# Performance work log

Measured on AMD Instinct MI355X. Metric: run time of the kernel, lower is better.

Reference implementation:

```python
import jax, jax.numpy as jnp
import numpy as np

B = 16; Hp = 24; Wp = 24; N = Hp * Wp + 2  # 578 = patches + cls + freq tokens
D = 768; H = 12; HDIM = D // H
BAND = 64; SD = 16  # sd = min(16, max(4, band_dim))
HID = 3072  # int(embed_dim * mlp_ratio)
SCALE = HDIM ** -0.5; CLIP = 10.0
FILM_SCALE = 0.5; SPEC_INIT = 0.02; GATE_INIT = 0.05


def _ln(x, w, b, eps=1e-6):
    m = jnp.mean(x, axis=-1, keepdims=True)
    v = jnp.mean((x - m) ** 2, axis=-1, keepdims=True)
    return (x - m) * jax.lax.rsqrt(v + eps) * w + b


def _rms(x, eps=1e-6):
    return x * jax.lax.rsqrt(jnp.mean(x * x, axis=-1, keepdims=True) + eps)


def setup_inputs() -> dict:
    key = jax.random.key(0)
    ks = jax.random.split(key, 16)
    rn = lambda k, s, sc=1.0: jax.random.normal(k, s, dtype=jnp.float32) * sc
    return {
        "x": rn(ks[0], (B, N, D)),
        "band_tokens": rn(ks[1], (B, 1, D)),  # unused by forward (matches torch signature)
        "freq_token_for_cond": rn(ks[2], (B, 1, D)),
        "freq_summary": rn(ks[3], (B, D)),
        "token_band_feat": rn(ks[4], (B, N, BAND)),
        "alpha": jnp.ones((1,), jnp.float32),
        "ln_gate_w": jnp.ones((D,), jnp.float32), "ln_gate_b": jnp.zeros((D,), jnp.float32),
        "film_w": rn(ks[5], (D, 2 * D), 1e-4), "film_b": jnp.zeros((2 * D,), jnp.float32),
        "ln_attn_w": jnp.ones((D,), jnp.float32), "ln_attn_b": jnp.zeros((D,), jnp.float32),
        "qkv_w": rn(ks[6], (D, 3 * D), 0.02), "qkv_b": jnp.zeros((3 * D,), jnp.float32),
        "proj_w": rn(ks[7], (D, D), 0.02), "proj_b": jnp.zeros((D,), jnp.float32),
        "spec_bias_scale": jnp.float32(SPEC_INIT),
        "gate_w": rn(ks[8], (D, H), 1e-4), "gate_b": jnp.zeros((H,), jnp.float32),
        "band_proj_w": rn(ks[9], (BAND, SD), 0.02),
        "ln_mlp_w": jnp.ones((D,), jnp.float32), "ln_mlp_b": jnp.zeros((D,), jnp.float32),
        "fc1_w": rn(ks[10], (D, HID), 0.02), "fc1_b": jnp.zeros((HID,), jnp.float32),
        "fc2_w": rn(ks[11], (HID, D), 0.02), "fc2_b": jnp.zeros((D,), jnp.float32),
        "dw_w": rn(ks[12], (HID, 1, 3, 3), 0.1), "dw_b": jnp.zeros((HID,), jnp.float32),
    }


def _forward(x, band_tokens, freq_token_for_cond, freq_summary, token_band_feat, alpha,
             ln_gate_w, ln_gate_b, film_w, film_b, ln_attn_w, ln_attn_b,
             qkv_w, qkv_b, proj_w, proj_b, spec_bias_scale, gate_w, gate_b, band_proj_w,
             ln_mlp_w, ln_mlp_b, fc1_w, fc1_b, fc2_w, fc2_b, dw_w, dw_b):
    a = alpha.reshape(())
    # --- FiLM gate on patch tokens (replaces patch, no residual) ---
    cls_freq = x[:, :2]
    patch = x[:, 2:]
    p = _ln(patch, ln_gate_w, ln_gate_b)
    gb = freq_summary @ film_w + film_b            # [B, 2D]
    gamma, beta = jnp.split(gb, 2, axis=-1)
    gamma = jnp.tanh(gamma) * FILM_SCALE
    beta = jnp.tanh(beta) * FILM_SCALE
    patch = p * (1.0 + a * gamma[:, None, :]) + a * beta[:, None, :]
    x = jnp.concatenate([cls_freq, patch], axis=1)
    # --- spectral-similarity attention ---
    xn = _ln(x, ln_attn_w, ln_attn_b)
    qkv = (xn @ qkv_w + qkv_b).reshape(B, N, 3, H, HDIM)
    q = _rms(qkv[:, :, 0].transpose(0, 2, 1, 3))   # [B,H,N,hd]
    k = _rms(qkv[:, :, 1].transpose(0, 2, 1, 3))
    v = qkv[:, :, 2].transpose(0, 2, 1, 3)
    logits = jnp.einsum('bhnd,bhmd->bhnm', q * SCALE, k)
    s = _rms(token_band_feat @ band_proj_w)        # [B,N,SD]
    ssim = jnp.einsum('bns,bms->bnm', s, s)        # [B,N,N]
    logits = jnp.clip(logits + a * spec_bias_scale * ssim[:, None], -CLIP, CLIP)
    attn = jax.nn.softmax(logits, axis=-1)
    out = jnp.einsum('bhnm,bhmd->bhnd', attn, v)
    g = jnp.tanh(freq_token_for_cond[:, 0] @ gate_w + gate_b) * GATE_INIT  # [B,H]
    out = out * (1.0 + a * g[:, :, None, None])
    out = out.transpose(0, 2, 1, 3).reshape(B, N, D)
    x = x + (out @ proj_w + proj_b)
    # --- conv MLP on patch tokens only ---
    cls_freq = x[:, :2]
    patch = x[:, 2:]
    h = jax.nn.gelu(_ln(patch, ln_mlp_w, ln_mlp_b) @ fc1_w + fc1_b, approximate=False)
    h = h.transpose(0, 2, 1).reshape(B, HID, Hp, Wp)
    h = jax.lax.conv_general_dilated(h, dw_w, (1, 1), 'SAME', feature_group_count=HID,
                                     dimension_numbers=('NCHW', 'OIHW', 'NCHW'))
    h = jax.nn.silu(h + dw_b[None, :, None, None])
    h = h.reshape(B, HID, Hp * Wp).transpose(0, 2, 1)
    patch = patch + (h @ fc2_w + fc2_b)
    return jnp.concatenate([cls_freq, patch], axis=1)


def reference(x, band_tokens, freq_token_for_cond, freq_summary, token_band_feat, alpha,
              ln_gate_w, ln_gate_b, film_w, film_b, ln_attn_w, ln_attn_b,
              qkv_w, qkv_b, proj_w, proj_b, spec_bias_scale, gate_w, gate_b, band_proj_w,
              ln_mlp_w, ln_mlp_b, fc1_w, fc1_b, fc2_w, fc2_b, dw_w, dw_b):
    return _forward(x, band_tokens, freq_token_for_cond, freq_summary, token_band_feat, alpha,
                    ln_gate_w, ln_gate_b, film_w, film_b, ln_attn_w, ln_attn_b,
                    qkv_w, qkv_b, proj_w, proj_b, spec_bias_scale, gate_w, gate_b, band_proj_w,
                    ln_mlp_w, ln_mlp_b, fc1_w, fc1_b, fc2_w, fc2_b, dw_w, dw_b)
```

## Files before the change

### kernel.cpp

```cpp
#include <hip/hip_runtime.h>
#include <hip/hip_bf16.h>

#define BATCH 16
#define NTOK 578
#define NTOKP 592
#define NP 576
#define PGRID 24
#define DIM 768
#define NH 12
#define HDIM 64
#define BAND 64
#define SDIM 16
#define HID 3072
#define SCALE 0.125f
#define CLIPV 10.0f
#define KHS 104
#define VTS 72
#define PLS 72

typedef __attribute__((ext_vector_type(8))) short bf16x8;
typedef __attribute__((ext_vector_type(4))) float f32x4;

__device__ __forceinline__ float b2f(short u) {
  union { float f; unsigned int i; } x;
  x.i = ((unsigned int)(unsigned short)u) << 16;
  return x.f;
}
__device__ __forceinline__ short f2b(float x) {
  __hip_bfloat16 h = __float2bfloat16(x);
  return *reinterpret_cast<short*>(&h);
}

__device__ __forceinline__ void gload16(const short* g, short* l) {
  __builtin_amdgcn_global_load_lds(
      (const __attribute__((address_space(1))) unsigned int*)g,
      (__attribute__((address_space(3))) unsigned int*)l, 16, 0, 0);
}

__device__ __forceinline__ int swz_wgid(int orig, int nwg) {
  int xcd = orig & 7, i = orig >> 3;
  int q = nwg >> 3, r = nwg & 7;
  return (xcd < r) ? xcd * (q + 1) + i : r * (q + 1) + (xcd - r) * q + i;
}

__device__ __forceinline__ void block_reduce2(float& a, float& b) {
  __shared__ float sm[8];
  #pragma unroll
  for (int o = 32; o > 0; o >>= 1) { a += __shfl_down(a, o); b += __shfl_down(b, o); }
  int lane = threadIdx.x & 63, w = threadIdx.x >> 6;
  __syncthreads();
  if (lane == 0) { sm[w] = a; sm[4 + w] = b; }
  __syncthreads();
  a = sm[0] + sm[1] + sm[2] + sm[3];
  b = sm[4] + sm[5] + sm[6] + sm[7];
}

__device__ __forceinline__ void tw_body(
    const float* __restrict__ W, short* __restrict__ Wt, int K, int N,
    int kblk, int nblk, float (*t)[33]) {
  int k0 = kblk * 32, n0 = nblk * 32;
  int tx = threadIdx.x & 31, ty = threadIdx.x >> 5;
  #pragma unroll
  for (int i = 0; i < 4; i++)
    t[ty + 8 * i][tx] = W[(size_t)(k0 + ty + 8 * i) * N + n0 + tx];
  __syncthreads();
  #pragma unroll
  for (int i = 0; i < 4; i++)
    Wt[(size_t)(n0 + ty + 8 * i) * K + k0 + tx] = f2b(t[tx][ty + 8 * i]);
}

__global__ __launch_bounds__(256) void prep_weights(
    const float* __restrict__ qkv_w, const float* __restrict__ proj_w,
    const float* __restrict__ fc1_w, const float* __restrict__ fc2_w,
    const float* __restrict__ dww,
    short* __restrict__ qkvT, short* __restrict__ projT,
    short* __restrict__ fc1T, short* __restrict__ fc2T, float* __restrict__ dwt) {
  __shared__ float t[32][33];
  int id = blockIdx.x;
  if (id < 1728) {
    tw_body(qkv_w, qkvT, 768, 2304, id % 24, id / 24, t);
  } else if (id < 2304) {
    int u = id - 1728; tw_body(proj_w, projT, 768, 768, u % 24, u / 24, t);
  } else if (id < 4608) {
    int u = id - 2304; tw_body(fc1_w, fc1T, 768, 3072, u % 24, u / 24, t);
  } else if (id < 6912) {
    int u = id - 4608; tw_body(fc2_w, fc2T, 3072, 768, u % 96, u / 96, t);
  } else {
    int i = (id - 6912) * 256 + threadIdx.x;
    if (i < 9 * HID) { int tt = i / HID, c = i - tt * HID; dwt[i] = dww[c * 9 + tt]; }
  }
}

__global__ __launch_bounds__(256) void transpose_v(
    const short* __restrict__ v, short* __restrict__ vT) {
  __shared__ short t[64][72];
  int bh = blockIdx.y;
  int n0 = blockIdx.x * 64;
  int tid = threadIdx.x;
  const short* vb = v + (size_t)bh * NTOK * HDIM;
  short* ob = vT + (size_t)bh * HDIM * NTOKP;
  {
    int r = tid >> 2, c0 = (tid & 3) * 16;
    int n = n0 + r;
    bf16x8 a0 = {0,0,0,0,0,0,0,0}, a1 = {0,0,0,0,0,0,0,0};
    if (n < NTOK) {
      a0 = *(const bf16x8*)(vb + (size_t)n * HDIM + c0);
      a1 = *(const bf16x8*)(vb + (size_t)n * HDIM + c0 + 8);
    }
    *(bf16x8*)(&t[r][c0]) = a0;
    *(bf16x8*)(&t[r][c0 + 8]) = a1;
  }
  __syncthreads();
  {
    int d = tid & 63, nc = tid >> 6;
    int nbase = n0 + nc * 16;
    short tmp[16];
    #pragma unroll
    for (int e = 0; e < 16; e++) tmp[e] = t[nc * 16 + e][d];
    if (nbase + 16 <= NTOK) {
      *(bf16x8*)(ob + (size_t)d * NTOKP + nbase) = *(bf16x8*)tmp;
      *(bf16x8*)(ob + (size_t)d * NTOKP + nbase + 8) = *(bf16x8*)(tmp + 8);
    } else {
      for (int e = 0; e < 16; e++)
        if (nbase + e < NTOK) ob[(size_t)d * NTOKP + nbase + e] = tmp[e];
    }
  }
}

__global__ __launch_bounds__(256) void film_kernel(
    const float* __restrict__ fsum, const float* __restrict__ film_w, const float* __restrict__ film_b,
    const float* __restrict__ ftc, const float* __restrict__ gate_w, const float* __restrict__ gate_b,
    float* __restrict__ gamma, float* __restrict__ beta, float* __restrict__ g) {
  int bid = blockIdx.x, tid = threadIdx.x;
  if (bid < 24) {
    __shared__ float fs[BATCH][DIM];
    for (int i = tid; i < BATCH * DIM; i += 256) fs[i / DIM][i - (i / DIM) * DIM] = fsum[i];
    __syncthreads();
    int col = bid * 64 + (tid & 63);
    int b0 = tid >> 6;
    float acc[4];
    float bv = film_b[col];
    #pragma unroll
    for (int i = 0; i < 4; i++) acc[i] = bv;
    for (int k = 0; k < DIM; k++) {
      float w = film_w[(size_t)k * 2 * DIM + col];
      #pragma unroll
      for (int i = 0; i < 4; i++) acc[i] += fs[b0 + 4 * i][k] * w;
    }
    #pragma unroll
    for (int i = 0; i < 4; i++) {
      int b = b0 + 4 * i;
      float t = tanhf(acc[i]) * 0.5f;
      if (col < DIM) gamma[b * DIM + col] = t;
      else beta[b * DIM + (col - DIM)] = t;
    }
  } else {
    int i2 = tid;
    if (i2 < BATCH * NH) {
      int b = i2 / NH, h = i2 - b * NH;
      float acc = gate_b[h];
      for (int i = 0; i < DIM; i++) acc += ftc[b * DIM + i] * gate_w[i * NH + h];
      g[i2] = tanhf(acc) * 0.05f;
    }
  }
}

__global__ __launch_bounds__(256) void ln_film_kernel(
    const float* __restrict__ x, const float* __restrict__ gamma, const float* __restrict__ beta,
    const float* __restrict__ gw, const float* __restrict__ gb,
    const float* __restrict__ aw, const float* __restrict__ ab,
    const float* __restrict__ alpha, float* __restrict__ xw, __hip_bfloat16* __restrict__ xn) {
  int row = blockIdx.x;
  int b = row / NTOK, n = row % NTOK;
  int tid = threadIdx.x;
  const float* xr = x + (size_t)row * DIM;
  float vals[3];
  #pragma unroll
  for (int j = 0; j < 3; j++) vals[j] = xr[tid + j * 256];
  if (n >= 2) {
    float s = vals[0] + vals[1] + vals[2];
    float ss = vals[0]*vals[0] + vals[1]*vals[1] + vals[2]*vals[2];
    block_reduce2(s, ss);
    float mean = s * (1.f / 768.f);
    float inv = rsqrtf(ss * (1.f / 768.f) - mean * mean + 1e-6f);
    float a = alpha[0];
    #pragma unroll
    for (int j = 0; j < 3; j++) {
      int d = tid + j * 256;
      float p = (vals[j] - mean) * inv * gw[d] + gb[d];
      vals[j] = p * (1.f + a * gamma[(size_t)b * DIM + d]) + a * beta[(size_t)b * DIM + d];
    }
  }
  float* xwr = xw + (size_t)row * DIM;
  #pragma unroll
  for (int j = 0; j < 3; j++) xwr[tid + j * 256] = vals[j];
  float s = vals[0] + vals[1] + vals[2];
  float ss = vals[0]*vals[0] + vals[1]*vals[1] + vals[2]*vals[2];
  block_reduce2(s, ss);
  float mean = s * (1.f / 768.f);
  float inv = rsqrtf(ss * (1.f / 768.f) - mean * mean + 1e-6f);
  __hip_bfloat16* xnr = xn + (size_t)row * DIM;
  #pragma unroll
  for (int j = 0; j < 3; j++) {
    int d = tid + j * 256;
    xnr[d] = __float2bfloat16((vals[j] - mean) * inv * aw[d] + ab[d]);
  }
}

__global__ __launch_bounds__(256) void band_s_kernel(
    const float* __restrict__ tbf, const float* __restrict__ bw, float* __restrict__ s) {
  int row = blockIdx.x * 4 + (threadIdx.x >> 6);
  int lane = threadIdx.x & 63;
  if (row >= BATCH * NTOK) return;
  const float* t = tbf + (size_t)row * BAND;
  float val = 0.f;
  if (lane < SDIM) {
    for (int i = 0; i < BAND; i++) val += t[i] * bw[i * SDIM + lane];
  }
  float ss = val * val;
  #pragma unroll
  for (int o = 8; o > 0; o >>= 1) ss += __shfl_xor(ss, o, 16);
  if (lane < SDIM) s[(size_t)row * SDIM + lane] = val * rsqrtf(ss * (1.f / 16.f) + 1e-6f);
}

__device__ __forceinline__ void stage_tile256(
    const short* __restrict__ A, const short* __restrict__ Wt, int K,
    int m0, int n0, int kt, short* Al, short* Bl, int wid, int lrow, int lcol) {
  #pragma unroll
  for (int it = 0; it < 4; it++) {
    int r0 = wid * 8 + it * 64;
    gload16(A + (size_t)(m0 + r0 + lrow) * K + kt + lcol, Al + r0 * 64);
  }
  #pragma unroll
  for (int it = 0; it < 2; it++) {
    int r0 = wid * 8 + it * 64;
    gload16(Wt + (size_t)(n0 + r0 + lrow) * K + kt + lcol, Bl + r0 * 64);
  }
}

__device__ __forceinline__ void compute_tile256(
    const short* Al, const short* Bl, f32x4 acc[4][4],
    int wr, int wc, int ln15, int kb) {
  #pragma unroll
  for (int kk = 0; kk < 2; kk++) {
    bf16x8 af[4], bfr[4];
    #pragma unroll
    for (int i = 0; i < 4; i++)
      af[i] = *(const bf16x8*)(Al + (wr * 64 + i * 16 + ln15) * 64 + kk * 32 + kb * 8);
    #pragma unroll
    for (int j = 0; j < 4; j++)
      bfr[j] = *(const bf16x8*)(Bl + (wc * 64 + j * 16 + ln15) * 64 + kk * 32 + kb * 8);
    #pragma unroll
    for (int i = 0; i < 4; i++)
      #pragma unroll
      for (int j = 0; j < 4; j++)
        acc[i][j] = __builtin_amdgcn_mfma_f32_16x16x32_bf16(af[i], bfr[j], acc[i][j], 0, 0, 0);
  }
}

__device__ __forceinline__ void mfma_core_256(
    const short* __restrict__ A, const short* __restrict__ Wt,
    int K, int m0, int n0, f32x4 acc[4][4], short* Al, short* Bl) {
  int tid = threadIdx.x, lane = tid & 63, wid = tid >> 6;
  int wr = wid >> 1, wc = wid & 1;
  int ln15 = lane & 15, kb = lane >> 4;
  int lrow = lane >> 3, lcol = (lane & 7) * 8;
  #pragma unroll
  for (int i = 0; i < 4; i++)
    #pragma unroll
    for (int j = 0; j < 4; j++) acc[i][j] = (f32x4){0.f, 0.f, 0.f, 0.f};
  for (int kt = 0; kt < K; kt += 64) {
    stage_tile256(A, Wt, K, m0, n0, kt, Al, Bl, wid, lrow, lcol);
    __syncthreads();
    compute_tile256(Al, Bl, acc, wr, wc, ln15, kb);
    __syncthreads();
  }
}

__device__ __forceinline__ void stage_tile(
    const short* __restrict__ A, const short* __restrict__ Wt, int K,
    int m0, int n0, int kt, short* Al, short* Bl, int wid, int lrow, int lcol) {
  #pragma unroll
  for (int it = 0; it < 4; it++) {
    int r0 = wid * 8 + it * 32;
    gload16(A + (size_t)(m0 + r0 + lrow) * K + kt + lcol, Al + r0 * 64);
    gload16(Wt + (size_t)(n0 + r0 + lrow) * K + kt + lcol, Bl + r0 * 64);
  }
}

__device__ __forceinline__ void stage_tile64(
    const short* __restrict__ A, const short* __restrict__ Wt, int K,
    int m0, int n0, int kt, short* Al, short* Bl, int wid, int lrow, int lcol) {
  #pragma unroll
  for (int it = 0; it < 2; it++) {
    int r0 = wid * 8 + it * 32;
    gload16(A + (size_t)(m0 + r0 + lrow) * K + kt + lcol, Al + r0 * 64);
  }
  #pragma unroll
  for (int it = 0; it < 4; it++) {
    int r0 = wid * 8 + it * 32;
    gload16(Wt + (size_t)(n0 + r0 + lrow) * K + kt + lcol, Bl + r0 * 64);
  }
}

__device__ __forceinline__ void compute_tile64(
    const short* Al, const short* Bl, f32x4 acc[4][2],
    int wid, int ln15, int kb) {
  #pragma unroll
  for (int kk = 0; kk < 2; kk++) {
    bf16x8 af[4], bfr[2];
    #pragma unroll
    for (int i = 0; i < 4; i++)
      af[i] = *(const bf16x8*)(Al + (i * 16 + ln15) * 64 + kk * 32 + kb * 8);
    #pragma unroll
    for (int j = 0; j < 2; j++)
      bfr[j] = *(const bf16x8*)(Bl + (wid * 32 + j * 16 + ln15) * 64 + kk * 32 + kb * 8);
    #pragma unroll
    for (int i = 0; i < 4; i++)
      #pragma unroll
      for (int j = 0; j < 2; j++)
        acc[i][j] = __builtin_amdgcn_mfma_f32_16x16x32_bf16(af[i], bfr[j], acc[i][j], 0, 0, 0);
  }
}

__device__ __forceinline__ void mfma_core_64(
    const short* __restrict__ A, const short* __restrict__ Wt,
    int K, int m0, int n0, f32x4 acc[4][2],
    short* Al0, short* Bl0, short* Al1, short* Bl1) {
  int tid = threadIdx.x, lane = tid & 63, wid = tid >> 6;
  int ln15 = lane & 15, kb = lane >> 4;
  int lrow = lane >> 3, lcol = (lane & 7) * 8;
  #pragma unroll
  for (int i = 0; i < 4; i++)
    #pragma unroll
    for (int j = 0; j < 2; j++) acc[i][j] = (f32x4){0.f, 0.f, 0.f, 0.f};
  stage_tile64(A, Wt, K, m0, n0, 0, Al0, Bl0, wid, lrow, lcol);
  __syncthreads();
  for (int kt = 0; kt < K; kt += 128) {
    if (kt + 64 < K)
      stage_tile64(A, Wt, K, m0, n0, kt + 64, Al1, Bl1, wid, lrow, lcol);
    compute_tile64(Al0, Bl0, acc, wid, ln15, kb);
    __syncthreads();
    if (kt + 128 < K)
      stage_tile64(A, Wt, K, m0, n0, kt + 128, Al0, Bl0, wid, lrow, lcol);
    if (kt + 64 < K)
      compute_tile64(Al1, Bl1, acc, wid, ln15, kb);
    __syncthreads();
  }
}

__global__ __launch_bounds__(512) void gemm_qkv(
    const short* __restrict__ A, const short* __restrict__ Wt, const float* __restrict__ bias,
    __hip_bfloat16* __restrict__ q, __hip_bfloat16* __restrict__ k, __hip_bfloat16* __restrict__ v) {
  __shared__ short Al[256 * 64], Bl[128 * 64];
  f32x4 acc[4][4];
  int wgid = swz_wgid(blockIdx.x, 37 * 18);
  int m0 = (wgid / 18) * 256, n0 = (wgid % 18) * 128;
  mfma_core_256(A, Wt, DIM, m0, n0, acc, Al, Bl);
  int tid = threadIdx.x, lane = tid & 63, wid = tid >> 6, wr = wid >> 1, wc = wid & 1;
  int ln15 = lane & 15, lq = lane >> 4;
  int colbase = n0 + wc * 64;
  int which = colbase / DIM;
  int rem = colbase - which * DIM;
  int h = rem >> 6;
  __hip_bfloat16* dst = (which == 0) ? q : ((which == 1) ? k : v);
  float fin_scale = (which == 0) ? SCALE : 1.0f;
  float bv[4];
  #pragma unroll
  for (int j = 0; j < 4; j++) bv[j] = bias[colbase + j * 16 + ln15];
  #pragma unroll
  for (int i = 0; i < 4; i++) {
    #pragma unroll
    for (int r = 0; r < 4; r++) {
      int m = m0 + wr * 64 + i * 16 + lq * 4 + r;
      float v4[4];
      #pragma unroll
      for (int j = 0; j < 4; j++) v4[j] = acc[i][j][r] + bv[j];
      float inv = fin_scale;
      if (which < 2) {
        float ss = v4[0]*v4[0] + v4[1]*v4[1] + v4[2]*v4[2] + v4[3]*v4[3];
        ss += __shfl_xor(ss, 1); ss += __shfl_xor(ss, 2);
        ss += __shfl_xor(ss, 4); ss += __shfl_xor(ss, 8);
        inv = rsqrtf(ss * (1.f / 64.f) + 1e-6f) * fin_scale;
      }
      if (m < BATCH * NTOK) {
        int b = m / NTOK, n = m - b * NTOK;
        __hip_bfloat16* orow = dst + (((size_t)b * NH + h) * NTOK + n) * HDIM;
        #pragma unroll
        for (int j = 0; j < 4; j++)
          orow[j * 16 + ln15] = __float2bfloat16(v4[j] * inv);
      }
    }
  }
}

__global__ __launch_bounds__(512) void attn_mfma(
    const short* __restrict__ q, const short* __restrict__ k,
    const short* __restrict__ vT, const float* __restrict__ s,
    const float* __restrict__ g, const float* __restrict__ alpha,
    const float* __restrict__ sbs, short* __restrict__ ao) {
  __shared__ short Kh[2][64 * KHS];
  __shared__ short Vt[2][64 * VTS];
  __shared__ short Pl[8][16 * PLS];
  int xcd = blockIdx.x & 7, idx = blockIdx.x >> 3;
  int bh = xcd * 24 + idx / 5;
  int n0 = (idx % 5) * 128;
  int b = bh / NH, h = bh - b * NH;
  int tid = threadIdx.x, lane = tid & 63, w = tid >> 6;
  int l15 = lane & 15, lg = lane >> 4;
  float a = alpha[0], c = a * sbs[0];
  const short* qb = q + (size_t)bh * NTOK * HDIM;
  const short* kb = k + (size_t)bh * NTOK * HDIM;
  const short* vtb = vT + (size_t)bh * HDIM * NTOKP;
  const float* sb = s + (size_t)b * NTOK * SDIM;
  const bf16x8 Z8 = {0, 0, 0, 0, 0, 0, 0, 0};

  int qrow = n0 + w * 16 + l15;
  int qsrc = (qrow < NTOK) ? qrow : 0;
  bf16x8 qf0 = *(const bf16x8*)(qb + (size_t)qsrc * HDIM + lg * 8);
  bf16x8 qf1 = *(const bf16x8*)(qb + (size_t)qsrc * HDIM + 32 + lg * 8);
  bf16x8 qf2 = Z8;
  if (lg < 2) {
    const float* sp = sb + (size_t)qsrc * SDIM + lg * 8;
    #pragma unroll
    for (int j = 0; j < 8; j++) qf2[j] = f2b(c * sp[j]);
  }

  f32x4 accO[4];
  #pragma unroll
  for (int dd = 0; dd < 4; dd++) accO[dd] = (f32x4){0.f, 0.f, 0.f, 0.f};
  float rsum[4] = {0.f, 0.f, 0.f, 0.f};

  int srow = (tid & 255) >> 2, sseg = tid & 3;
  if (tid < 256 && sseg == 3) {
    #pragma unroll
    for (int bb = 0; bb < 2; bb++) {
      short* dst = Kh[bb] + srow * KHS + 80;
      *(bf16x8*)dst = Z8;
      *(bf16x8*)(dst + 8) = Z8;
    }
  }

  auto stage = [&](int mt, short* KhB, short* VtB) {
    if (tid < 256) {
      int key = mt + srow;
      bool kok = key < NTOK;
      if (sseg < 2) {
        bf16x8 v0 = Z8, v1 = Z8, v2 = Z8, v3 = Z8;
        if (kok) {
          const short* src = kb + (size_t)key * HDIM + sseg * 32;
          v0 = *(const bf16x8*)(src);
          v1 = *(const bf16x8*)(src + 8);
          v2 = *(const bf16x8*)(src + 16);
          v3 = *(const bf16x8*)(src + 24);
        }
        short* dst = KhB + srow * KHS + sseg * 32;
        *(bf16x8*)dst = v0;
        *(bf16x8*)(dst + 8) = v1;
        *(bf16x8*)(dst + 16) = v2;
        *(bf16x8*)(dst + 24) = v3;
      } else if (sseg == 2) {
        bf16x8 v0 = Z8, v1 = Z8;
        if (kok) {
          const float* sp = sb + (size_t)key * SDIM;
          #pragma unroll
          for (int j = 0; j < 8; j++) { v0[j] = f2b(sp[j]); v1[j] = f2b(sp[j + 8]); }
        }
        short* dst = KhB + srow * KHS + 64;
        *(bf16x8*)dst = v0;
        *(bf16x8*)(dst + 8) = v1;
      }
    } else {
      int kk0 = sseg * 16;
      short* dst = VtB + srow * VTS + kk0;
      const short* src = vtb + (size_t)srow * NTOKP + mt + kk0;
      if (mt + kk0 + 16 <= NTOK) {
        *(bf16x8*)dst = *(const bf16x8*)src;
        *(bf16x8*)(dst + 8) = *(const bf16x8*)(src + 8);
      } else {
        for (int e = 0; e < 16; e++)
          dst[e] = (mt + kk0 + e < NTOK) ? src[e] : (short)0;
      }
    }
  };

  stage(0, Kh[0], Vt[0]);
  __syncthreads();
  const int NT = 10;
  for (int ti = 0; ti < NT; ti++) {
    int mt = ti * 64, cur = ti & 1;
    if (ti + 1 < NT) stage(mt + 64, Kh[cur ^ 1], Vt[cur ^ 1]);
    const short* KhC = Kh[cur];
    const short* VtC = Vt[cur];
    f32x4 sa[4];
    __builtin_amdgcn_s_setprio(1);
    #pragma unroll
    for (int jj = 0; jj < 4; jj++) {
      sa[jj] = (f32x4){0.f, 0.f, 0.f, 0.f};
      const short* kp = KhC + (jj * 16 + l15) * KHS + lg * 8;
      sa[jj] = __builtin_amdgcn_mfma_f32_16x16x32_bf16(qf0, *(const bf16x8*)kp, sa[jj], 0, 0, 0);
      sa[jj] = __builtin_amdgcn_mfma_f32_16x16x32_bf16(qf1, *(const bf16x8*)(kp + 32), sa[jj], 0, 0, 0);
      sa[jj] = __builtin_amdgcn_mfma_f32_16x16x32_bf16(qf2, *(const bf16x8*)(kp + 64), sa[jj], 0, 0, 0);
    }
    __builtin_amdgcn_s_setprio(0);
    short* pw = Pl[w];
    float ps[4][4];
    #pragma unroll
    for (int jj = 0; jj < 4; jj++) {
      bool ok = (mt + jj * 16 + l15) < NTOK;
      #pragma unroll
      for (int r = 0; r < 4; r++) {
        float x = sa[jj][r];
        x = fminf(fmaxf(x, -CLIPV), CLIPV);
        float e = ok ? __expf(x) : 0.f;
        ps[jj][r] = e;
        pw[(lg * 4 + r) * PLS + jj * 16 + l15] = f2b(e);
      }
    }
    #pragma unroll
    for (int r = 0; r < 4; r++) {
      float t = ps[0][r] + ps[1][r] + ps[2][r] + ps[3][r];
      t += __shfl_xor(t, 1); t += __shfl_xor(t, 2);
      t += __shfl_xor(t, 4); t += __shfl_xor(t, 8);
      rsum[r] += t;
    }
    __builtin_amdgcn_s_setprio(1);
    #pragma unroll
    for (int kc = 0; kc < 2; kc++) {
      bf16x8 pa = *(const bf16x8*)(pw + l15 * PLS + kc * 32 + lg * 8);
      #pragma unroll
      for (int dd = 0; dd < 4; dd++) {
        bf16x8 vf = *(const bf16x8*)(VtC + (dd * 16 + l15) * VTS + kc * 32 + lg * 8);
        accO[dd] = __builtin_amdgcn_mfma_f32_16x16x32_bf16(pa, vf, accO[dd], 0, 0, 0);
      }
    }
    __builtin_amdgcn_s_setprio(0);
    __syncthreads();
  }
  float gm = 1.f + a * g[bh];
  #pragma unroll
  for (int r = 0; r < 4; r++) {
    int n = n0 + w * 16 + lg * 4 + r;
    if (n >= NTOK) continue;
    float inv = gm / rsum[r];
    short* orow = ao + ((size_t)b * NTOK + n) * DIM + h * HDIM;
    #pragma unroll
    for (int dd = 0; dd < 4; dd++)
      orow[dd * 16 + l15] = f2b(accO[dd][r] * inv);
  }
}

__global__ __launch_bounds__(256) void gemm_proj(
    const short* __restrict__ A, const short* __restrict__ Wt, const float* __restrict__ bias,
    float* __restrict__ xw, float* __restrict__ out) {
  __shared__ short Al[2 * 64 * 64], Bl[2 * 128 * 64];
  f32x4 acc[4][2];
  int wgid = swz_wgid(blockIdx.x, 145 * 6);
  int m0 = (wgid / 6) * 64, n0 = (wgid % 6) * 128;
  mfma_core_64(A, Wt, DIM, m0, n0, acc, Al, Bl, Al + 64 * 64, Bl + 128 * 64);
  int tid = threadIdx.x, lane = tid & 63, wid = tid >> 6;
  int ln15 = lane & 15, lq = lane >> 4;
  #pragma unroll
  for (int i = 0; i < 4; i++) {
    #pragma unroll
    for (int j = 0; j < 2; j++) {
      int col = n0 + wid * 32 + j * 16 + ln15;
      float bv = bias[col];
      #pragma unroll
      for (int r = 0; r < 4; r++) {
        int m = m0 + i * 16 + lq * 4 + r;
        if (m >= BATCH * NTOK) continue;
        int n = m % NTOK;
        float val = acc[i][j][r] + bv + xw[(size_t)m * DIM + col];
        xw[(size_t)m * DIM + col] = val;
        if (n < 2) out[(size_t)m * DIM + col] = val;
      }
    }
  }
}

__global__ __launch_bounds__(256) void ln_mlp_kernel(
    const float* __restrict__ x2, const float* __restrict__ w, const float* __restrict__ bb,
    __hip_bfloat16* __restrict__ xm) {
  int r = blockIdx.x;
  int b = r / NP, pi = r % NP;
  int tid = threadIdx.x;
  const float* xr = x2 + ((size_t)b * NTOK + 2 + pi) * DIM;
  float vals[3];
  #pragma unroll
  for (int j = 0; j < 3; j++) vals[j] = xr[tid + j * 256];
  float s = vals[0] + vals[1] + vals[2];
  float ss = vals[0]*vals[0] + vals[1]*vals[1] + vals[2]*vals[2];
  block_reduce2(s, ss);
  float mean = s * (1.f / 768.f);
  float inv = rsqrtf(ss * (1.f / 768.f) - mean * mean + 1e-6f);
  __hip_bfloat16* xo = xm + (size_t)r * DIM;
  #pragma unroll
  for (int j = 0; j < 3; j++) {
    int d = tid + j * 256;
    xo[d] = __float2bfloat16((vals[j] - mean) * inv * w[d] + bb[d]);
  }
}

__global__ __launch_bounds__(512) void gemm_fc1(
    const short* __restrict__ A, const short* __restrict__ Wt, const float* __restrict__ bias,
    __hip_bfloat16* __restrict__ h1) {
  __shared__ short Al[256 * 64], Bl[128 * 64];
  f32x4 acc[4][4];
  int wgid = swz_wgid(blockIdx.x, 18 * 24);
  int m0 = (wgid / 24) * 256, n0 = (wgid % 24) * 128;
  mfma_core_256(A, Wt, DIM, m0, n0, acc, Al, Bl);
  int tid = threadIdx.x, lane = tid & 63, wid = tid >> 6, wr = wid >> 1, wc = wid & 1;
  int ln15 = lane & 15, lq = lane >> 4;
  #pragma unroll
  for (int i = 0; i < 4; i++) {
    #pragma unroll
    for (int j = 0; j < 4; j++) {
      int col = n0 + wc * 64 + j * 16 + ln15;
      float bv = bias[col];
      #pragma unroll
      for (int r = 0; r < 4; r++) {
        int m = m0 + wr * 64 + i * 16 + lq * 4 + r;
        float val = acc[i][j][r] + bv;
        float ge = 0.5f * val * (1.f + erff(val * 0.70710678118f));
        h1[(size_t)m * HID + col] = __float2bfloat16(ge);
      }
    }
  }
}

__global__ __launch_bounds__(256) void dwconv_kernel(
    const __hip_bfloat16* __restrict__ h1, const float* __restrict__ dwt,
    const float* __restrict__ dwb, __hip_bfloat16* __restrict__ h2) {
  int gx = blockIdx.x;
  int b = gx / 144, g = gx - b * 144;
  int y = g / 6, x0 = (g - y * 6) * 4;
  int tid = threadIdx.x;
  int c0 = blockIdx.y * 512 + (tid & 63) * 8;
  int x = x0 + (tid >> 6);
  const short* in = (const short*)h1 + (size_t)b * NP * HID + c0;
  bf16x8 iv[3][3];
  #pragma unroll
  for (int ky = 0; ky < 3; ky++) {
    int yy = y + ky - 1;
    #pragma unroll
    for (int kx = 0; kx < 3; kx++) {
      int xx = x + kx - 1;
      bool ok = (yy >= 0 && yy < PGRID && xx >= 0 && xx < PGRID);
      iv[ky][kx] = ok ? *(const bf16x8*)(in + (size_t)(yy * PGRID + xx) * HID)
                      : (bf16x8){0, 0, 0, 0, 0, 0, 0, 0};
    }
  }
  float acc[8];
  {
    float4 b0 = *(const float4*)(dwb + c0);
    float4 b1 = *(const float4*)(dwb + c0 + 4);
    acc[0] = b0.x; acc[1] = b0.y; acc[2] = b0.z; acc[3] = b0.w;
    acc[4] = b1.x; acc[5] = b1.y; acc[6] = b1.z; acc[7] = b1.w;
  }
  #pragma unroll
  for (int t = 0; t < 9; t++) {
    float4 w0 = *(const float4*)(dwt + t * HID + c0);
    float4 w1 = *(const float4*)(dwt + t * HID + c0 + 4);
    bf16x8 xv = iv[t / 3][t % 3];
    acc[0] += b2f(xv[0]) * w0.x; acc[1] += b2f(xv[1]) * w0.y;
    acc[2] += b2f(xv[2]) * w0.z; acc[3] += b2f(xv[3]) * w0.w;
    acc[4] += b2f(xv[4]) * w1.x; acc[5] += b2f(xv[5]) * w1.y;
    acc[6] += b2f(xv[6]) * w1.z; acc[7] += b2f(xv[7]) * w1.w;
  }
  short ov[8];
  #pragma unroll
  for (int e = 0; e < 8; e++) {
    float v = acc[e];
    ov[e] = f2b(v / (1.f + __expf(-v)));
  }
  *(bf16x8*)((short*)h2 + ((size_t)b * NP + y * PGRID + x) * HID + c0) = *(bf16x8*)ov;
}

__global__ __launch_bounds__(256) void gemm_fc2(
    const short* __restrict__ A, const short* __restrict__ Wt, const float* __restrict__ bias,
    const float* __restrict__ xw, float* __restrict__ out, int b0) {
  __shared__ short Al[2 * 64 * 64], Bl[2 * 128 * 64];
  f32x4 acc[4][2];
  int wgid = swz_wgid(blockIdx.x, 72 * 6);
  int m0 = (wgid / 6) * 64, n0 = (wgid % 6) * 128;
  mfma_core_64(A, Wt, HID, m0, n0, acc, Al, Bl, Al + 64 * 64, Bl + 128 * 64);
  int tid = threadIdx.x, lane = tid & 63, wid = tid >> 6;
  int ln15 = lane & 15, lq = lane >> 4;
  #pragma unroll
  for (int i = 0; i < 4; i++) {
    #pragma unroll
    for (int j = 0; j < 2; j++) {
      int col = n0 + wid * 32 + j * 16 + ln15;
      float bv = bias[col];
      #pragma unroll
      for (int r = 0; r < 4; r++) {
        int m = m0 + i * 16 + lq * 4 + r;
        int bl = m / NP, pi = m - bl * NP;
        size_t orow = ((size_t)(b0 + bl) * NTOK + 2 + pi) * DIM;
        out[orow + col] = acc[i][j][r] + bv + xw[orow + col];
      }
    }
  }
}

extern "C" void kernel_launch(void* const* d_in, const int* in_sizes, int n_in,
                              void* d_out, int out_size, void* d_ws, size_t ws_size,
                              hipStream_t stream) {
  const float* x      = (const float*)d_in[0];
  const float* ftc    = (const float*)d_in[2];
  const float* fsum   = (const float*)d_in[3];
  const float* tbf    = (const float*)d_in[4];
  const float* alpha  = (const float*)d_in[5];
  const float* lgw    = (const float*)d_in[6];
  const float* lgb    = (const float*)d_in[7];
  const float* film_w = (const float*)d_in[8];
  const float* film_b = (const float*)d_in[9];
  const float* law    = (const float*)d_in[10];
  const float* lab    = (const float*)d_in[11];
  const float* qkv_w  = (const float*)d_in[12];
  const float* qkv_b  = (const float*)d_in[13];
  const float* proj_w = (const float*)d_in[14];
  const float* proj_b = (const float*)d_in[15];
  const float* sbs    = (const float*)d_in[16];
  const float* gate_w = (const float*)d_in[17];
  const float* gate_b = (const float*)d_in[18];
  const float* band_w = (const float*)d_in[19];
  const float* lmw    = (const float*)d_in[20];
  const float* lmb    = (const float*)d_in[21];
  const float* fc1_w  = (const float*)d_in[22];
  const float* fc1_b  = (const float*)d_in[23];
  const float* fc2_w  = (const float*)d_in[24];
  const float* fc2_b  = (const float*)d_in[25];
  const float* dw_w   = (const float*)d_in[26];
  const float* dw_b   = (const float*)d_in[27];
  float* out = (float*)d_out;

  float* ws = (float*)d_ws;
  const size_t SZ = (size_t)BATCH * NTOK * DIM;

  float* p_xw = ws;
  short* p_xn = (short*)(ws + SZ);
  short* p_q  = (short*)(ws + SZ + SZ / 2);
  short* p_k  = (short*)(ws + 2 * SZ);
  short* p_v  = (short*)(ws + 2 * SZ + SZ / 2);
  float* p_s  = ws + 3 * SZ;
  float* p_gamma = p_s + (size_t)BATCH * NTOK * SDIM;
  float* p_beta  = p_gamma + BATCH * DIM;
  float* p_g     = p_beta + BATCH * DIM;
  float* p_dwt   = p_g + 256;
  float* wtb = p_dwt + 9 * HID;
  short* qkvT = (short*)wtb;
  short* projT = qkvT + (size_t)768 * 2304;
  short* fc1T  = projT + (size_t)768 * 768;
  short* fc2T  = fc1T + (size_t)768 * 3072;
  short* h2c   = fc2T + (size_t)3072 * 768;

  const size_t total_floats =
      3 * SZ + (size_t)BATCH * NTOK * SDIM + 2 * (size_t)BATCH * DIM + 256 + 9 * HID +
      ((size_t)768 * 2304 + 768 * 768 + 768 * 3072 + 3072 * 768) / 2 +
      ((size_t)8 * NP * HID) / 2;
  if (ws_size < total_floats * sizeof(float)) return;

  short* p_ao = p_xn;
  short* p_xm = p_q;
  short* h1c  = p_k;
  short* p_vT = h2c;

  dim3 blk(256);

  prep_weights<<<dim3(7020), blk, 0, stream>>>(
      qkv_w, proj_w, fc1_w, fc2_w, dw_w, qkvT, projT, fc1T, fc2T, p_dwt);

  film_kernel<<<dim3(25), blk, 0, stream>>>(
      fsum, film_w, film_b, ftc, gate_w, gate_b, p_gamma, p_beta, p_g);

  ln_film_kernel<<<dim3(BATCH * NTOK), blk, 0, stream>>>(
      x, p_gamma, p_beta, lgw, lgb, law, lab, alpha, p_xw, (__hip_bfloat16*)p_xn);

  band_s_kernel<<<dim3((BATCH * NTOK + 3) / 4), blk, 0, stream>>>(tbf, band_w, p_s);

  gemm_qkv<<<dim3(37 * 18), dim3(512), 0, stream>>>(
      p_xn, qkvT, qkv_b, (__hip_bfloat16*)p_q, (__hip_bfloat16*)p_k, (__hip_bfloat16*)p_v);

  transpose_v<<<dim3(10, BATCH * NH), blk, 0, stream>>>(p_v, p_vT);

  attn_mfma<<<dim3(960), dim3(512), 0, stream>>>(
      p_q, p_k, p_vT, p_s, p_g, alpha, sbs, p_ao);

  gemm_proj<<<dim3(145 * 6), blk, 0, stream>>>(p_ao, projT, proj_b, p_xw, out);

  ln_mlp_kernel<<<dim3(BATCH * NP), blk, 0, stream>>>(p_xw, lmw, lmb, (__hip_bfloat16*)p_xm);

  for (int cc = 0; cc < 2; cc++) {
    const short* Ach = p_xm + (size_t)cc * 4608 * DIM;
    gemm_fc1<<<dim3(18 * 24), dim3(512), 0, stream>>>(Ach, fc1T, fc1_b, (__hip_bfloat16*)h1c);
    dwconv_kernel<<<dim3(8 * 144, 6), blk, 0, stream>>>(
        (const __hip_bfloat16*)h1c, p_dwt, dw_b, (__hip_bfloat16*)h2c);
    gemm_fc2<<<dim3(72 * 6), blk, 0, stream>>>(h2c, fc2T, fc2_b, p_xw, out, cc * 8);
  }
}
```

Measured before the change: 517.3 us.

## Rework weight transpose, split film/gate kernels, remap GEMM tile order

The weight-prep transpose now uses 256x64 tiles with float4 loads, bf16 conversion into shared memory and 16-byte vector stores, replacing 32x32 fp32 tiles with scalar stores. The film projection is vectorised with float4 weight loads over fewer blocks, and the per-head gate computation moves to its own kernel using a wave-level reduction. All four GEMMs swap their block-to-tile mapping so consecutive workgroups walk along M within the same N column, which is meant to improve reuse of weight tiles in cache. Shared buffers in the 64-row GEMMs are declared as separate arrays, and one unused helper is removed.

Result: slower. 558.3 us (+7.9%).

```diff
diff --git a/kernel.cpp b/kernel.cpp
--- a/kernel.cpp
+++ b/kernel.cpp
@@ -55,18 +55,29 @@
   b = sm[4] + sm[5] + sm[6] + sm[7];
 }
 
-__device__ __forceinline__ void tw_body(
+#define TKS 266
+__device__ __forceinline__ void tw2(
     const float* __restrict__ W, short* __restrict__ Wt, int K, int N,
-    int kblk, int nblk, float (*t)[33]) {
-  int k0 = kblk * 32, n0 = nblk * 32;
-  int tx = threadIdx.x & 31, ty = threadIdx.x >> 5;
-  #pragma unroll
-  for (int i = 0; i < 4; i++)
-    t[ty + 8 * i][tx] = W[(size_t)(k0 + ty + 8 * i) * N + n0 + tx];
+    int kblk, int nblk, short* t) {
+  int tid = threadIdx.x;
+  int k0 = kblk * 256, n0 = nblk * 64;
+  int r0 = tid >> 4, c0 = (tid & 15) * 4;
+  #pragma unroll
+  for (int it = 0; it < 16; it++) {
+    int r = it * 16 + r0;
+    float4 v = *(const float4*)(W + (size_t)(k0 + r) * N + n0 + c0);
+    t[(c0 + 0) * TKS + r] = f2b(v.x);
+    t[(c0 + 1) * TKS + r] = f2b(v.y);
+    t[(c0 + 2) * TKS + r] = f2b(v.z);
+    t[(c0 + 3) * TKS + r] = f2b(v.w);
+  }
   __syncthreads();
-  #pragma unroll
-  for (int i = 0; i < 4; i++)
-    Wt[(size_t)(n0 + ty + 8 * i) * K + k0 + tx] = f2b(t[tx][ty + 8 * i]);
+  int n1 = tid >> 5, k1 = (tid & 31) * 8;
+  #pragma unroll
+  for (int it = 0; it < 8; it++) {
+    int n = it * 8 + n1;
+    *(bf16x8*)(Wt + (size_t)(n0 + n) * K + k0 + k1) = *(bf16x8*)(t + n * TKS + k1);
+  }
 }
 
 __global__ __launch_bounds__(256) void prep_weights(
@@ -75,20 +86,83 @@
     const float* __restrict__ dww,
     short* __restrict__ qkvT, short* __restrict__ projT,
     short* __restrict__ fc1T, short* __restrict__ fc2T, float* __restrict__ dwt) {
-  __shared__ float t[32][33];
+  __shared__ short t[64 * TKS];
   int id = blockIdx.x;
-  if (id < 1728) {
-    tw_body(qkv_w, qkvT, 768, 2304, id % 24, id / 24, t);
-  } else if (id < 2304) {
-    int u = id - 1728; tw_body(proj_w, projT, 768, 768, u % 24, u / 24, t);
-  } else if (id < 4608) {
-    int u = id - 2304; tw_body(fc1_w, fc1T, 768, 3072, u % 24, u / 24, t);
-  } else if (id < 6912) {
-    int u = id - 4608; tw_body(fc2_w, fc2T, 3072, 768, u % 96, u / 96, t);
+  if (id < 108) {
+    tw2(qkv_w, qkvT, 768, 2304, id % 3, id / 3, t);
+  } else if (id < 144) {
+    int u = id - 108; tw2(proj_w, projT, 768, 768, u % 3, u / 3, t);
+  } else if (id < 288) {
+    int u = id - 144; tw2(fc1_w, fc1T, 768, 3072, u % 3, u / 3, t);
+  } else if (id < 432) {
+    int u = id - 288; tw2(fc2_w, fc2T, 3072, 768, u % 12, u / 12, t);
   } else {
-    int i = (id - 6912) * 256 + threadIdx.x;
+    int i = (id - 432) * 256 + threadIdx.x;
     if (i < 9 * HID) { int tt = i / HID, c = i - tt * HID; dwt[i] = dww[c * 9 + tt]; }
   }
+}
+
+__global__ __launch_bounds__(256) void film_kernel(
+    const float* __restrict__ fsum, const float* __restrict__ film_w,
+    const float* __restrict__ film_b, float* __restrict__ gamma, float* __restrict__ beta) {
+  __shared__ float fs[BATCH][DIM];
+  int tid = threadIdx.x;
+  for (int i = tid; i < BATCH * DIM; i += 256) fs[i / DIM][i - (i / DIM) * DIM] = fsum[i];
+  __syncthreads();
+  int col4 = blockIdx.x * 128 + (tid & 31) * 4;
+  int bq = tid >> 5;
+  float4 bv = *(const float4*)(film_b + col4);
+  float a0[4] = {bv.x, bv.y, bv.z, bv.w};
+  float a1[4] = {bv.x, bv.y, bv.z, bv.w};
+  #pragma unroll 4
+  for (int k = 0; k < DIM; k++) {
+    float4 w = *(const float4*)(film_w + (size_t)k * 2 * DIM + col4);
+    float f0 = fs[bq][k], f1 = fs[bq + 8][k];
+    a0[0] += f0 * w.x; a0[1] += f0 * w.y; a0[2] += f0 * w.z; a0[3] += f0 * w.w;
+    a1[0] += f1 * w.x; a1[1] += f1 * w.y; a1[2] += f1 * w.z; a1[3] += f1 * w.w;
+  }
+  #pragma unroll
+  for (int ci = 0; ci < 4; ci++) {
+    int col = col4 + ci;
+    float t0 = tanhf(a0[ci]) * 0.5f, t1 = tanhf(a1[ci]) * 0.5f;
+    if (col < DIM) {
+      gamma[bq * DIM + col] = t0;
+      gamma[(bq + 8) * DIM + col] = t1;
+    } else {
+      beta[bq * DIM + (col - DIM)] = t0;
+      beta[(bq + 8) * DIM + (col - DIM)] = t1;
+    }
+  }
+}
+
+__global__ __launch_bounds__(256) void gate_kernel(
+    const float* __restrict__ ftc, const float* __restrict__ gate_w,
+    const float* __restrict__ gate_b, float* __restrict__ g) {
+  int widx = blockIdx.x * 4 + (threadIdx.x >> 6);
+  int lane = threadIdx.x & 63;
+  if (widx >= BATCH * NH) return;
+  int b = widx / NH, h = widx - b * NH;
+  float acc = 0.f;
+  for (int k = lane; k < DIM; k += 64) acc += ftc[b * DIM + k] * gate_w[k * NH + h];
+  #pragma unroll
+  for (int o = 32; o > 0; o >>= 1) acc += __shfl_down(acc, o);
+  if (lane == 0) g[widx] = tanhf(acc + gate_b[h]) * 0.05f;
+}
+
+__global__ __launch_bounds__(256) void band_s_kernel(
+    const float* __restrict__ tbf, const float* __restrict__ bw, float* __restrict__ s) {
+  int row = blockIdx.x * 4 + (threadIdx.x >> 6);
+  int lane = threadIdx.x & 63;
+  if (row >= BATCH * NTOK) return;
+  const float* t = tbf + (size_t)row * BAND;
+  float val = 0.f;
+  if (lane < SDIM) {
+    for (int i = 0; i < BAND; i++) val += t[i] * bw[i * SDIM + lane];
+  }
+  float ss = val * val;
+  #pragma unroll
+  for (int o = 8; o > 0; o >>= 1) ss += __shfl_xor(ss, o, 16);
+  if (lane < SDIM) s[(size_t)row * SDIM + lane] = val * rsqrtf(ss * (1.f / 16.f) + 1e-6f);
 }
 
 __global__ __launch_bounds__(256) void transpose_v(
@@ -127,44 +201,6 @@
   }
 }
 
-__global__ __launch_bounds__(256) void film_kernel(
-    const float* __restrict__ fsum, const float* __restrict__ film_w, const float* __restrict__ film_b,
-    const float* __restrict__ ftc, const float* __restrict__ gate_w, const float* __restrict__ gate_b,
-    float* __restrict__ gamma, float* __restrict__ beta, float* __restrict__ g) {
-  int bid = blockIdx.x, tid = threadIdx.x;
-  if (bid < 24) {
-    __shared__ float fs[BATCH][DIM];
-    for (int i = tid; i < BATCH * DIM; i += 256) fs[i / DIM][i - (i / DIM) * DIM] = fsum[i];
-    __syncthreads();
-    int col = bid * 64 + (tid & 63);
-    int b0 = tid >> 6;
-    float acc[4];
-    float bv = film_b[col];
-    #pragma unroll
-    for (int i = 0; i < 4; i++) acc[i] = bv;
-    for (int k = 0; k < DIM; k++) {
-      float w = film_w[(size_t)k * 2 * DIM + col];
-      #pragma unroll
-      for (int i = 0; i < 4; i++) acc[i] += fs[b0 + 4 * i][k] * w;
-    }
-    #pragma unroll
-    for (int i = 0; i < 4; i++) {
-      int b = b0 + 4 * i;
-      float t = tanhf(acc[i]) * 0.5f;
-      if (col < DIM) gamma[b * DIM + col] = t;
-      else beta[b * DIM + (col - DIM)] = t;
-    }
-  } else {
-    int i2 = tid;
-    if (i2 < BATCH * NH) {
-      int b = i2 / NH, h = i2 - b * NH;
-      float acc = gate_b[h];
-      for (int i = 0; i < DIM; i++) acc += ftc[b * DIM + i] * gate_w[i * NH + h];
-      g[i2] = tanhf(acc) * 0.05f;
-    }
-  }
-}
-
 __global__ __launch_bounds__(256) void ln_film_kernel(
     const float* __restrict__ x, const float* __restrict__ gamma, const float* __restrict__ beta,
     const float* __restrict__ gw, const float* __restrict__ gb,
@@ -207,22 +243,6 @@
   }
 }
 
-__global__ __launch_bounds__(256) void band_s_kernel(
-    const float* __restrict__ tbf, const float* __restrict__ bw, float* __restrict__ s) {
-  int row = blockIdx.x * 4 + (threadIdx.x >> 6);
-  int lane = threadIdx.x & 63;
-  if (row >= BATCH * NTOK) return;
-  const float* t = tbf + (size_t)row * BAND;
-  float val = 0.f;
-  if (lane < SDIM) {
-    for (int i = 0; i < BAND; i++) val += t[i] * bw[i * SDIM + lane];
-  }
-  float ss = val * val;
-  #pragma unroll
-  for (int o = 8; o > 0; o >>= 1) ss += __shfl_xor(ss, o, 16);
-  if (lane < SDIM) s[(size_t)row * SDIM + lane] = val * rsqrtf(ss * (1.f / 16.f) + 1e-6f);
-}
-
 __device__ __forceinline__ void stage_tile256(
     const short* __restrict__ A, const short* __restrict__ Wt, int K,
     int m0, int n0, int kt, short* Al, short* Bl, int wid, int lrow, int lcol) {
@@ -274,17 +294,6 @@
     __syncthreads();
     compute_tile256(Al, Bl, acc, wr, wc, ln15, kb);
     __syncthreads();
-  }
-}
-
-__device__ __forceinline__ void stage_tile(
-    const short* __restrict__ A, const short* __restrict__ Wt, int K,
-    int m0, int n0, int kt, short* Al, short* Bl, int wid, int lrow, int lcol) {
-  #pragma unroll
-  for (int it = 0; it < 4; it++) {
-    int r0 = wid * 8 + it * 32;
-    gload16(A + (size_t)(m0 + r0 + lrow) * K + kt + lcol, Al + r0 * 64);
-    gload16(Wt + (size_t)(n0 + r0 + lrow) * K + kt + lcol, Bl + r0 * 64);
   }
 }
 
@@ -355,7 +364,7 @@
   __shared__ short Al[256 * 64], Bl[128 * 64];
   f32x4 acc[4][4];
   int wgid = swz_wgid(blockIdx.x, 37 * 18);
-  int m0 = (wgid / 18) * 256, n0 = (wgid % 18) * 128;
+  int m0 = (wgid % 37) * 256, n0 = (wgid / 37) * 128;
   mfma_core_256(A, Wt, DIM, m0, n0, acc, Al, Bl);
   int tid = threadIdx.x, lane = tid & 63, wid = tid >> 6, wr = wid >> 1, wc = wid & 1;
   int ln15 = lane & 15, lq = lane >> 4;
@@ -553,11 +562,11 @@
 __global__ __launch_bounds__(256) void gemm_proj(
     const short* __restrict__ A, const short* __restrict__ Wt, const float* __restrict__ bias,
     float* __restrict__ xw, float* __restrict__ out) {
-  __shared__ short Al[2 * 64 * 64], Bl[2 * 128 * 64];
+  __shared__ short Al0[64 * 64], Bl0[128 * 64], Al1[64 * 64], Bl1[128 * 64];
   f32x4 acc[4][2];
   int wgid = swz_wgid(blockIdx.x, 145 * 6);
-  int m0 = (wgid / 6) * 64, n0 = (wgid % 6) * 128;
-  mfma_core_64(A, Wt, DIM, m0, n0, acc, Al, Bl, Al + 64 * 64, Bl + 128 * 64);
+  int m0 = (wgid % 145) * 64, n0 = (wgid / 145) * 128;
+  mfma_core_64(A, Wt, DIM, m0, n0, acc, Al0, Bl0, Al1, Bl1);
   int tid = threadIdx.x, lane = tid & 63, wid = tid >> 6;
   int ln15 = lane & 15, lq = lane >> 4;
   #pragma unroll
@@ -608,7 +617,7 @@
   __shared__ short Al[256 * 64], Bl[128 * 64];
   f32x4 acc[4][4];
   int wgid = swz_wgid(blockIdx.x, 18 * 24);
-  int m0 = (wgid / 24) * 256, n0 = (wgid % 24) * 128;
+  int m0 = (wgid % 18) * 256, n0 = (wgid / 18) * 128;
   mfma_core_256(A, Wt, DIM, m0, n0, acc, Al, Bl);
   int tid = threadIdx.x, lane = tid & 63, wid = tid >> 6, wr = wid >> 1, wc = wid & 1;
   int ln15 = lane & 15, lq = lane >> 4;
@@ -680,11 +689,11 @@
 __global__ __launch_bounds__(256) void gemm_fc2(
     const short* __restrict__ A, const short* __restrict__ Wt, const float* __restrict__ bias,
     const float* __restrict__ xw, float* __restrict__ out, int b0) {
-  __shared__ short Al[2 * 64 * 64], Bl[2 * 128 * 64];
+  __shared__ short Al0[64 * 64], Bl0[128 * 64], Al1[64 * 64], Bl1[128 * 64];
   f32x4 acc[4][2];
   int wgid = swz_wgid(blockIdx.x, 72 * 6);
-  int m0 = (wgid / 6) * 64, n0 = (wgid % 6) * 128;
-  mfma_core_64(A, Wt, HID, m0, n0, acc, Al, Bl, Al + 64 * 64, Bl + 128 * 64);
+  int m0 = (wgid % 72) * 64, n0 = (wgid / 72) * 128;
+  mfma_core_64(A, Wt, HID, m0, n0, acc, Al0, Bl0, Al1, Bl1);
   int tid = threadIdx.x, lane = tid & 63, wid = tid >> 6;
   int ln15 = lane & 15, lq = lane >> 4;
   #pragma unroll
@@ -769,16 +778,17 @@
 
   dim3 blk(256);
 
-  prep_weights<<<dim3(7020), blk, 0, stream>>>(
+  prep_weights<<<dim3(432 + 108), blk, 0, stream>>>(
       qkv_w, proj_w, fc1_w, fc2_w, dw_w, qkvT, projT, fc1T, fc2T, p_dwt);
 
-  film_kernel<<<dim3(25), blk, 0, stream>>>(
-      fsum, film_w, film_b, ftc, gate_w, gate_b, p_gamma, p_beta, p_g);
+  film_kernel<<<dim3(12), blk, 0, stream>>>(fsum, film_w, film_b, p_gamma, p_beta);
+
+  gate_kernel<<<dim3(48), blk, 0, stream>>>(ftc, gate_w, gate_b, p_g);
+
+  band_s_kernel<<<dim3((BATCH * NTOK + 3) / 4), blk, 0, stream>>>(tbf, band_w, p_s);
 
   ln_film_kernel<<<dim3(BATCH * NTOK), blk, 0, stream>>>(
       x, p_gamma, p_beta, lgw, lgb, law, lab, alpha, p_xw, (__hip_bfloat16*)p_xn);
-
-  band_s_kernel<<<dim3((BATCH * NTOK + 3) / 4), blk, 0, stream>>>(tbf, band_w, p_s);
 
   gemm_qkv<<<dim3(37 * 18), dim3(512), 0, stream>>>(
       p_xn, qkvT, qkv_b, (__hip_bfloat16*)p_q, (__hip_bfloat16*)p_k, (__hip_bfloat16*)p_v);
```
